# Kernel optimization log

Hardware: AMD Instinct MI355X
Metric: run time of the kernel (lower is better)

Reference implementation:

```python
import jax, jax.numpy as jnp
import numpy as np

N_USER = 1_000_000
N_FEED = 1_000_000
DIM = 100
BATCH = 16384
MU = 0.5


def setup_inputs() -> dict:
    key = jax.random.key(0)
    k1, k2, k3, k4, k5, k6 = jax.random.split(key, 6)
    users = jax.random.randint(k1, (BATCH,), 0, N_USER)
    feeds = jax.random.randint(k2, (BATCH,), 0, N_FEED)
    user_latent = jax.random.normal(k3, (N_USER, DIM), dtype=jnp.float32) * 0.02
    feed_latent = jax.random.normal(k4, (N_FEED, DIM), dtype=jnp.float32) * 0.02
    user_bias = jax.random.normal(k5, (N_USER,), dtype=jnp.float32) * 0.5
    feed_bias = jax.random.normal(k6, (N_FEED,), dtype=jnp.float32) * 0.5
    return {
        "users": users,
        "feeds": feeds,
        "user_latent": user_latent,
        "feed_latent": feed_latent,
        "user_bias": user_bias,
        "feed_bias": feed_bias,
    }


def reference(users, feeds, user_latent, feed_latent, user_bias, feed_bias):
    # gather latent factors and biases
    u = user_latent[users]          # [B, D]
    f = feed_latent[feeds]          # [B, D]
    ub = user_bias[users]           # [B]
    fb = feed_bias[feeds]           # [B]
    # diag(u @ f.T) == rowwise dot product; compute it directly (same math,
    # avoids the O(B^2 D) blowup of the original torch code)
    dot = jnp.sum(u * f, axis=-1)   # [B]
    return dot + ub + fb + MU
```

## Files before the change

kernel.cpp:

```cpp
#include <hip/hip_runtime.h>
#include <hip/hip_bf16.h>

#define MF_BATCH 16384
#define MF_DIM 100
#define MF_MU 0.5f

__global__ __launch_bounds__(256) void Matrixfactorization_39350490366306_kernel(
    const int* __restrict__ users,
    const int* __restrict__ feeds,
    const float* __restrict__ user_latent,
    const float* __restrict__ feed_latent,
    const float* __restrict__ user_bias,
    const float* __restrict__ feed_bias,
    float* __restrict__ out,
    int batch) {
  const int gtid = blockIdx.x * blockDim.x + threadIdx.x;
  const int row  = gtid >> 6;
  const int lane = threadIdx.x & 63;
  if (row >= batch) return;

  const int u = users[row];
  const int f = feeds[row];

  float partial = 0.0f;
  if (lane < MF_DIM / 2) {
    const float2 a = reinterpret_cast<const float2*>(
        user_latent + (size_t)u * MF_DIM)[lane];
    const float2 b = reinterpret_cast<const float2*>(
        feed_latent + (size_t)f * MF_DIM)[lane];
    partial = a.x * b.x + a.y * b.y;
  }

  #pragma unroll
  for (int off = 32; off > 0; off >>= 1)
    partial += __shfl_down(partial, off, 64);

  if (lane == 0) {
    out[row] = partial + user_bias[u] + feed_bias[f] + MF_MU;
  }
}

extern "C" void kernel_launch(void* const* d_in, const int* in_sizes, int n_in,
                              void* d_out, int out_size, void* d_ws, size_t ws_size,
                              hipStream_t stream) {
  const int*   users       = (const int*)d_in[0];
  const int*   feeds       = (const int*)d_in[1];
  const float* user_latent = (const float*)d_in[2];
  const float* feed_latent = (const float*)d_in[3];
  const float* user_bias   = (const float*)d_in[4];
  const float* feed_bias   = (const float*)d_in[5];
  float* out = (float*)d_out;

  const int batch = in_sizes[0];
  const int waves_per_block = 256 / 64;
  const int grid = (batch + waves_per_block - 1) / waves_per_block;

  Matrixfactorization_39350490366306_kernel<<<grid, 256, 0, stream>>>(
      users, feeds, user_latent, feed_latent, user_bias, feed_bias, out, batch);
}
```

Before: 9.674 us.

## Process two rows per wavefront with float4 loads and in-reduction bias fetch

Each 64-lane wave now handles two batch rows, 32 lanes per row, and loads latent vectors as float4 instead of float2. The bias loads are issued in parallel by spare lanes 25 and 26 and folded into the xor-shuffle reduction, which is shortened to five steps. This halves the grid and puts more lanes to work on each wave, cutting the serial bias loads after the reduction. The int2 index loads and the absence of a second-row bounds check assume an even batch size.

```diff
diff --git a/kernel.cpp b/kernel.cpp
--- a/kernel.cpp
+++ b/kernel.cpp
@@ -1,7 +1,6 @@
 #include <hip/hip_runtime.h>
 #include <hip/hip_bf16.h>
 
-#define MF_BATCH 16384
 #define MF_DIM 100
 #define MF_MU 0.5f
 
@@ -14,29 +13,39 @@
     const float* __restrict__ feed_bias,
     float* __restrict__ out,
     int batch) {
-  const int gtid = blockIdx.x * blockDim.x + threadIdx.x;
-  const int row  = gtid >> 6;
-  const int lane = threadIdx.x & 63;
-  if (row >= batch) return;
+  const int tid    = blockIdx.x * blockDim.x + threadIdx.x;
+  const int wave   = tid >> 6;
+  const int lane   = threadIdx.x & 63;
+  const int half   = lane >> 5;
+  const int sublane = lane & 31;
 
-  const int u = users[row];
-  const int f = feeds[row];
+  const int row0 = wave * 2;
+  if (row0 >= batch) return;
+
+  const int2 uu = reinterpret_cast<const int2*>(users)[wave];
+  const int2 ff = reinterpret_cast<const int2*>(feeds)[wave];
+  const int u = half ? uu.y : uu.x;
+  const int f = half ? ff.y : ff.x;
 
   float partial = 0.0f;
-  if (lane < MF_DIM / 2) {
-    const float2 a = reinterpret_cast<const float2*>(
-        user_latent + (size_t)u * MF_DIM)[lane];
-    const float2 b = reinterpret_cast<const float2*>(
-        feed_latent + (size_t)f * MF_DIM)[lane];
-    partial = a.x * b.x + a.y * b.y;
+  if (sublane < MF_DIM / 4) {
+    const float4 a = reinterpret_cast<const float4*>(
+        user_latent + (size_t)u * MF_DIM)[sublane];
+    const float4 b = reinterpret_cast<const float4*>(
+        feed_latent + (size_t)f * MF_DIM)[sublane];
+    partial = a.x * b.x + a.y * b.y + a.z * b.z + a.w * b.w;
+  } else if (sublane == 25) {
+    partial = user_bias[u];
+  } else if (sublane == 26) {
+    partial = feed_bias[f];
   }
 
   #pragma unroll
-  for (int off = 32; off > 0; off >>= 1)
-    partial += __shfl_down(partial, off, 64);
+  for (int off = 16; off > 0; off >>= 1)
+    partial += __shfl_xor(partial, off, 64);
 
-  if (lane == 0) {
-    out[row] = partial + user_bias[u] + feed_bias[f] + MF_MU;
+  if (sublane == 0) {
+    out[row0 + half] = partial + MF_MU;
   }
 }
 
@@ -52,8 +61,8 @@
   float* out = (float*)d_out;
 
   const int batch = in_sizes[0];
-  const int waves_per_block = 256 / 64;
-  const int grid = (batch + waves_per_block - 1) / waves_per_block;
+  const int rows_per_block = 8;
+  const int grid = (batch + rows_per_block - 1) / rows_per_block;
 
   Matrixfactorization_39350490366306_kernel<<<grid, 256, 0, stream>>>(
       users, feeds, user_latent, feed_latent, user_bias, feed_bias, out, batch);
```

Result: faster. 9.333 us (-3.5%).
